# Optimization experiments

Measured on AMD Instinct MI355X. Metric: run time of the kernel, lower is better.

Reference implementation:

```python
import jax, jax.numpy as jnp
import numpy as np


def _sqdist(X1, X2):
    # squared euclidean distance matrix, matches torch.cdist(...,p=2)**2
    d2 = (jnp.sum(X1 * X1, -1)[:, None] + jnp.sum(X2 * X2, -1)[None, :]
          - 2.0 * (X1 @ X2.T))
    return jnp.maximum(d2, 0.0)


def setup_inputs() -> dict:
    key = jax.random.key(0)
    k1, k2, k3, k4, k5, k6 = jax.random.split(key, 6)
    n, m, d, C = 1024, 2048, 4, 64
    X_train = jax.random.normal(k1, (n, d), dtype=jnp.float32)
    y_train = jax.random.normal(k2, (n,), dtype=jnp.float32)
    X_test = jax.random.normal(k3, (m, d), dtype=jnp.float32)
    # positive params within the priors' supports
    lengthscale = jax.random.uniform(k4, (C,), minval=0.1, maxval=3.0, dtype=jnp.float32)
    variance = jax.random.uniform(k5, (C,), minval=0.1, maxval=3.0, dtype=jnp.float32)
    noise = jax.random.uniform(k6, (C,), minval=0.01, maxval=0.5, dtype=jnp.float32)
    return {"X_train": X_train, "y_train": y_train, "X_test": X_test,
            "lengthscale": lengthscale, "variance": variance, "noise": noise}


def reference(X_train, y_train, X_test, lengthscale, variance, noise):
    n = X_train.shape[0]
    ls2 = (lengthscale ** 2)[:, None, None]          # [C,1,1]
    var = variance[:, None, None]                     # [C,1,1]
    d2_tr = _sqdist(X_train, X_train)                 # [n,n]
    d2_te = _sqdist(X_test, X_train)                  # [m,n]
    K_train = var * jnp.exp(-0.5 * d2_tr[None] / ls2)   # [C,n,n]
    K_test = var * jnp.exp(-0.5 * d2_te[None] / ls2)    # [C,m,n]
    K_noisy = K_train + noise[:, None, None] * jnp.eye(n, dtype=K_train.dtype)
    L = jnp.linalg.cholesky(K_noisy)                  # batched [C,n,n]

    def per_chain(Lc, Ktc):
        solve = jax.scipy.linalg.solve_triangular
        z = solve(Lc, y_train, lower=True)            # [n]
        alpha = solve(Lc, z, lower=True, trans=1)     # [n]
        pred_mean = Ktc @ alpha                       # [m]
        v = solve(Lc, Ktc.T, lower=True)              # [n,m]
        pred_var = jnp.sum(v * v, axis=0)             # [m]
        return pred_mean, pred_var

    means, vars_ = jax.vmap(per_chain)(L, K_test)     # [C,m] each
    return means.mean(axis=0), vars_.mean(axis=0)
```

## Files before the change

kernel.cpp:

```cpp
#include <hip/hip_runtime.h>
#include <hip/hip_fp16.h>
#include <math.h>

#define N 1024
#define M 2048
#define C 64
#define NB 128
#define TB 8
#define NBLK 36
#define PL ((size_t)NBLK*NB*NB)

typedef __attribute__((ext_vector_type(8))) short bf16x8;
typedef __attribute__((ext_vector_type(8))) _Float16 f16x8;
typedef __attribute__((ext_vector_type(4))) float f32x4;

__device__ __forceinline__ size_t pblk(int ib, int jt){
    return ((size_t)((ib*(ib+1))/2 + jt))*((size_t)NB*NB);
}

#define TT(r,c) T[(r)][(((c)+(r)) & 127)]


__device__ __forceinline__ float sqdist4(const float4 a, const float4 b){
    float dx=a.x-b.x, dy=a.y-b.y, dz=a.z-b.z, dw=a.w-b.w;
    return dx*dx+dy*dy+dz*dz+dw*dw;
}

__device__ __forceinline__ void split4(float x0, float x1, float x2, float x3,
                                       uint2& hi, uint2& lo){
    unsigned b0=__float_as_uint(x0), b1=__float_as_uint(x1),
             b2=__float_as_uint(x2), b3=__float_as_uint(x3);
    unsigned h0=b0&0xFFFF0000u, h1=b1&0xFFFF0000u, h2=b2&0xFFFF0000u, h3=b3&0xFFFF0000u;
    hi.x = (h0>>16)|h1;  hi.y = (h2>>16)|h3;
    float l0=x0-__uint_as_float(h0), l1=x1-__uint_as_float(h1),
          l2=x2-__uint_as_float(h2), l3=x3-__uint_as_float(h3);
    lo.x = (__float_as_uint(l0)>>16) | (__float_as_uint(l1)&0xFFFF0000u);
    lo.y = (__float_as_uint(l2)>>16) | (__float_as_uint(l3)&0xFFFF0000u);
}

__device__ void chol_invert_lds(float T[NB][NB], int tid){
    for (int j = 0; j < NB; j++){
        float d = TT(j,j);
        float inv = 1.0f / sqrtf(d);
        for (int i = j+1+tid; i < NB; i += 256) TT(i,j) *= inv;
        if (tid == 0) TT(j,j) = d * inv;
        __syncthreads();
        int i = j+1 + (tid >> 1);
        if (i < NB){
            float lij = TT(i,j);
            for (int k = j+1+(tid&1); k <= i; k += 2)
                TT(i,k) -= lij * TT(k,j);
        }
        __syncthreads();
    }
    for (int i = 0; i < NB; i++){
        float inv_ii = 1.0f / TT(i,i);
        int j = tid & 127, hi = tid >> 7;
        float S = 0.0f;
        if (j < i){
            for (int k = i-1-hi; k >= j; k -= 2)
                S += TT(i,k) * TT(k,j);
        }
        if (hi && j < i) TT(j,i) = S;
        __syncthreads();
        if (!hi){
            if (j < i)      TT(i,j) = -inv_ii * (S + TT(j,i));
            else if (j == i) TT(i,i) = inv_ii;
        }
        __syncthreads();
    }
}


struct FragLds { __half Ah[4096], Al[4096], Bh[4096], Bl[4096]; };
struct SmX { float4 xr[NB]; float4 xc[NB]; };
union SmU { FragLds f; float T[NB][NB]; SmX x; };

__device__ __forceinline__ void stage_f16(__half* __restrict__ Hh, __half* __restrict__ Hl,
                                          const float* __restrict__ S, int ld,
                                          int k0, bool contig, int tid){
    #pragma unroll
    for (int h = 0; h < 2; h++){
        int u = tid + h*256;
        int fr = u & 15, kg = (u>>4)&3, rt = (u>>6)&3, hf = u>>8;
        int rc = hf*64 + rt*16 + fr;
        int kk = k0 + kg*8;
        float x[8];
        if (contig){
            float4 v0 = *(const float4*)&S[(size_t)rc*ld + kk];
            float4 v1 = *(const float4*)&S[(size_t)rc*ld + kk + 4];
            x[0]=v0.x;x[1]=v0.y;x[2]=v0.z;x[3]=v0.w;
            x[4]=v1.x;x[5]=v1.y;x[6]=v1.z;x[7]=v1.w;
        } else {
            #pragma unroll
            for (int e=0;e<8;e++) x[e] = S[(size_t)(kk+e)*ld + rc];
        }
        union { __half h[8]; uint4 u4; } Hi, Lo;
        #pragma unroll
        for (int e=0;e<8;e++){
            __half hv = __float2half_rn(x[e]);
            Hi.h[e] = hv;
            Lo.h[e] = __float2half_rn(x[e] - __half2float(hv));
        }
        *(uint4*)&Hh[(size_t)u*8] = Hi.u4;
        *(uint4*)&Hl[(size_t)u*8] = Lo.u4;
    }
}

__device__ __forceinline__ void mfma_slab_f16(const __half* Ah, const __half* Al,
                                              const __half* Bh, const __half* Bl,
                                              int wrow, int wcol, int lane,
                                              f32x4 acc[4][4]){
    f16x8 ah[4], al[4];
    #pragma unroll
    for (int rt=0;rt<4;rt++){
        ah[rt] = *(const f16x8*)&Ah[((size_t)((wrow*4+rt)*64 + lane))*8];
        al[rt] = *(const f16x8*)&Al[((size_t)((wrow*4+rt)*64 + lane))*8];
    }
    #pragma unroll
    for (int ct=0;ct<4;ct++){
        f16x8 bh = *(const f16x8*)&Bh[((size_t)((wcol*4+ct)*64 + lane))*8];
        f16x8 bl = *(const f16x8*)&Bl[((size_t)((wcol*4+ct)*64 + lane))*8];
        #pragma unroll
        for (int rt=0;rt<4;rt++){
            f32x4 a = acc[rt][ct];
            a = __builtin_amdgcn_mfma_f32_16x16x32_f16(ah[rt], bh, a, 0,0,0);
            a = __builtin_amdgcn_mfma_f32_16x16x32_f16(ah[rt], bl, a, 0,0,0);
            a = __builtin_amdgcn_mfma_f32_16x16x32_f16(al[rt], bh, a, 0,0,0);
            acc[rt][ct] = a;
        }
    }
}

__device__ void gemm_f16_unit(const float* __restrict__ A, int lda,
                              const float* __restrict__ B, int ldb, bool bContig,
                              FragLds& F, f32x4 acc[4][4], int tid){
    int lane = tid & 63, w = tid >> 6, wrow = w>>1, wcol = w&1;
    for (int k0 = 0; k0 < NB; k0 += 32){
        __syncthreads();
        stage_f16(F.Ah, F.Al, A, lda, k0, true, tid);
        stage_f16(F.Bh, F.Bl, B, ldb, k0, bContig, tid);
        __syncthreads();
        mfma_slab_f16(F.Ah, F.Al, F.Bh, F.Bl, wrow, wcol, lane, acc);
    }
}

__device__ __forceinline__ void store_f16acc(float* __restrict__ Cp, int ldc,
                                             const f32x4 acc[4][4], float sgn, int tid){
    int lane = tid&63, w = tid>>6, wrow = w>>1, wcol = w&1;
    int fr = lane&15, kg = lane>>4;
    #pragma unroll
    for (int rt=0;rt<4;rt++)
      #pragma unroll
      for (int ct=0;ct<4;ct++)
        #pragma unroll
        for (int r=0;r<4;r++){
            int row = wrow*64 + rt*16 + kg*4 + r;
            int col = wcol*64 + ct*16 + fr;
            Cp[(size_t)row*ldc + col] = sgn*acc[rt][ct][r];
        }
}

#define ZERO_ACC(acc) { _Pragma("unroll") for (int zi=0;zi<4;zi++) _Pragma("unroll") for (int zj=0;zj<4;zj++) acc[zi][zj] = (f32x4)0.0f; }


__global__ void k_init_acc(float* __restrict__ acc){
    int i = blockIdx.x*blockDim.x + threadIdx.x;
    if (i < 2*M) acc[i] = 0.0f;
}

__global__ void k_build_d2te(const float* __restrict__ Xtr, const float* __restrict__ Xte,
                             float* __restrict__ d2){
    int j = blockIdx.x;
    float4 xj = ((const float4*)Xte)[j];
    for (int i = threadIdx.x; i < N; i += blockDim.x){
        float4 xi = ((const float4*)Xtr)[i];
        d2[(size_t)j*N + i] = sqdist4(xi,xj);
    }
}

__global__ void k_final(const float* __restrict__ acc, float* __restrict__ out){
    int i = blockIdx.x*blockDim.x + threadIdx.x;
    if (i < 2*M) out[i] = acc[i] * (1.0f/64.0f);
}

__global__ __launch_bounds__(256) void k_build_K(const float* __restrict__ Xtr,
                          const float* __restrict__ ls,
                          const float* __restrict__ var, const float* __restrict__ noise,
                          float* __restrict__ Lbuf){
    __shared__ SmU sm;
    int c = blockIdx.y, flat = blockIdx.x;
    int ib = 0; while ((ib+1)*(ib+2)/2 <= flat) ib++;
    int jt = flat - ib*(ib+1)/2;
    int tid = threadIdx.x;
    if (tid < NB) sm.x.xr[tid] = ((const float4*)Xtr)[ib*NB + tid];
    else          sm.x.xc[tid-NB] = ((const float4*)Xtr)[jt*NB + (tid-NB)];
    __syncthreads();
    float il2 = 1.0f/(ls[c]*ls[c]);
    float vc = var[c], nc = noise[c];
    float* blk = Lbuf + c*PL + pblk(ib,jt);
    for (int idx = tid; idx < NB*NB; idx += 256){
        int r = idx >> 7, col = idx & 127;
        float d2v = sqdist4(sm.x.xr[r], sm.x.xc[col]);
        float v = vc*__expf(-0.5f*d2v*il2);
        if (ib==jt && r==col) v += nc;
        blk[idx] = v;
    }
    if (flat == 0){
        __threadfence_block();
        __syncthreads();
        float (*T)[NB] = sm.T;
        for (int idx = tid; idx < NB*NB; idx += 256){
            int r = idx >> 7, col = idx & 127;
            TT(r,col) = blk[idx];
        }
        __syncthreads();
        chol_invert_lds(T, tid);
        for (int idx = tid; idx < NB*NB; idx += 256){
            int r = idx >> 7, col = idx & 127;
            blk[idx] = (col <= r) ? TT(r,col) : 0.0f;
        }
    }
}

__global__ __launch_bounds__(256) void k_panel(float* __restrict__ Lbuf, int kb){
    __shared__ FragLds F;
    int c = blockIdx.x;
    int ib = kb + 1 + blockIdx.y;
    int tid = threadIdx.x;
    float* base = Lbuf + (size_t)c*PL;
    float* Ablk = base + pblk(ib,kb);
    const float* Dv = base + pblk(kb,kb);
    f32x4 acc[4][4]; ZERO_ACC(acc);
    gemm_f16_unit(Ablk, NB, Dv, NB, true, F, acc, tid);
    store_f16acc(Ablk, NB, acc, 1.0f, tid);
}

__global__ __launch_bounds__(256) void k_syrk(float* __restrict__ Lbuf, int kb){
    __shared__ SmU sm;
    int c = blockIdx.x;
    int flat = blockIdx.y;
    int di = 0; while ((di+1)*(di+2)/2 <= flat) di++;
    int dj = flat - di*(di+1)/2;
    int i = kb+1+di, j = kb+1+dj;
    int tid = threadIdx.x;
    float* base = Lbuf + (size_t)c*PL;
    float* Cblk = base + pblk(i,j);
    const float* Ablk = base + pblk(i,kb);
    const float* Bblk = base + pblk(j,kb);
    f32x4 acc[4][4]; ZERO_ACC(acc);
    gemm_f16_unit(Ablk, NB, Bblk, NB, true, sm.f, acc, tid);
    int lane = tid&63, w = tid>>6, wrow = w>>1, wcol = w&1;
    int fr = lane&15, kg = lane>>4;
    if (flat != 0){
        #pragma unroll
        for (int rt=0;rt<4;rt++)
          #pragma unroll
          for (int ct=0;ct<4;ct++)
            #pragma unroll
            for (int r=0;r<4;r++){
                int row = wrow*64 + rt*16 + kg*4 + r;
                int col = wcol*64 + ct*16 + fr;
                Cblk[(size_t)row*NB + col] -= acc[rt][ct][r];
            }
    } else {
        __syncthreads();
        float (*T)[NB] = sm.T;
        #pragma unroll
        for (int rt=0;rt<4;rt++)
          #pragma unroll
          for (int ct=0;ct<4;ct++)
            #pragma unroll
            for (int r=0;r<4;r++){
                int row = wrow*64 + rt*16 + kg*4 + r;
                int col = wcol*64 + ct*16 + fr;
                TT(row,col) = Cblk[(size_t)row*NB + col] - acc[rt][ct][r];
            }
        __syncthreads();
        chol_invert_lds(T, tid);
        for (int idx = tid; idx < NB*NB; idx += 256){
            int r = idx >> 7, col = idx & 127;
            Cblk[idx] = (col <= r) ? TT(r,col) : 0.0f;
        }
    }
}

__global__ __launch_bounds__(256) void k_gemmA(float* __restrict__ Trow,
                                               const float* __restrict__ Lbuf, int ib){
    __shared__ FragLds F;
    int c = blockIdx.x, ct = blockIdx.y;
    int tid = threadIdx.x;
    const float* base = Lbuf + (size_t)c*PL;
    const float* Dv = base + pblk(ib,ib);
    const float* Bsrc = base + pblk(ib,ct);
    f32x4 acc[4][4]; ZERO_ACC(acc);
    gemm_f16_unit(Dv, NB, Bsrc, NB, false, F, acc, tid);
    store_f16acc(Trow + (size_t)c*NB*N + ct*NB, N, acc, 1.0f, tid);
}

__global__ __launch_bounds__(256) void k_gemmB(float* __restrict__ Lbuf,
                                               const float* __restrict__ Trow, int ib){
    __shared__ FragLds F;
    int c = blockIdx.x, jt = blockIdx.y;
    int tid = threadIdx.x;
    const float* G = Trow + (size_t)c*NB*N;
    float* base = Lbuf + (size_t)c*PL;
    f32x4 acc[4][4]; ZERO_ACC(acc);
    for (int kt = jt; kt < ib; kt++)
        gemm_f16_unit(G + kt*NB, N, base + pblk(kt,jt), NB, false, F, acc, tid);
    store_f16acc(base + pblk(ib,jt), NB, acc, -1.0f, tid);
}

__global__ void k_zvec(const float* __restrict__ Lbuf, const float* __restrict__ y,
                       float* __restrict__ z){
    int c = blockIdx.x;
    int p = blockIdx.y * 4 + (threadIdx.x >> 6);
    int lane = threadIdx.x & 63;
    int pb = p >> 7, pl = p & 127;
    const float* base = Lbuf + (size_t)c*PL;
    float s = 0.0f;
    for (int kt = 0; kt <= pb; kt++){
        const float* row = base + pblk(pb,kt) + (size_t)pl*NB;
        int lim = (kt==pb) ? pl : NB-1;
        for (int i = lane; i <= lim; i += 64) s += row[i]*y[kt*NB + i];
    }
    for (int off = 32; off; off >>= 1) s += __shfl_down(s, off);
    if (lane == 0) z[c*N + p] = s;
}

__global__ __launch_bounds__(256) void k_wsplit(float* __restrict__ Lbuf){
    int c = blockIdx.y, flat = blockIdx.x;
    int tid = threadIdx.x;
    float* blk = Lbuf + c*PL + (size_t)flat*NB*NB;
    float4 v[16];
    #pragma unroll
    for (int h = 0; h < 8; h++){
        int g = tid + h*256;
        int u = g & 511, slab = g >> 9;
        int fr = u&15, kg = (u>>4)&3, rt = (u>>6)&3, hf = u>>8;
        int row = hf*64 + rt*16 + fr;
        int k = slab*32 + kg*8;
        v[2*h]   = *(const float4*)&blk[(size_t)row*NB + k];
        v[2*h+1] = *(const float4*)&blk[(size_t)row*NB + k + 4];
    }
    __syncthreads();
    unsigned short* out = (unsigned short*)blk;
    #pragma unroll
    for (int h = 0; h < 8; h++){
        int g = tid + h*256;
        int u = g & 511, slab = g >> 9;
        uint2 h0, l0, h1, l1;
        split4(v[2*h].x, v[2*h].y, v[2*h].z, v[2*h].w, h0, l0);
        split4(v[2*h+1].x, v[2*h+1].y, v[2*h+1].z, v[2*h+1].w, h1, l1);
        *(uint4*)&out[((size_t)(slab*2+0)*512 + u)*8] = make_uint4(h0.x,h0.y,h1.x,h1.y);
        *(uint4*)&out[((size_t)(slab*2+1)*512 + u)*8] = make_uint4(l0.x,l0.y,l1.x,l1.y);
    }
}

__global__ __launch_bounds__(256) void k_bigg(const float* __restrict__ Lbuf,
                                              const float* __restrict__ d2,
                                              const float* __restrict__ zbuf,
                                              const float* __restrict__ ls,
                                              const float* __restrict__ var,
                                              float* __restrict__ acc_out){
    __shared__ unsigned short Ah[4096], Al[4096], Bh[4096], Bl[4096];
    int flat = blockIdx.x, c = blockIdx.y;
    int jt = flat & 15;
    int pt = ((flat >> 4) + (jt & 7)) & 7;
    int tid = threadIdx.x;
    int lane = tid & 63, w = tid >> 6;
    int wrow = w >> 1, wcol = w & 1;
    float il2 = 1.0f/(ls[c]*ls[c]);
    float vc = var[c];
    float ec = -0.5f*il2;
    const float* Arow = d2 + (size_t)(jt*NB)*N;
    const float* Wbase = Lbuf + (size_t)c*PL;
    int klen = (pt+1)*NB;
    f32x4 acc[4][4]; ZERO_ACC(acc);

    int fr = lane & 15, kg = lane >> 4;
    int q = tid & 7, rs = tid >> 3;
    int kgq = q >> 1, e4 = (q & 1) * 4;

    for (int k0 = 0; k0 < klen; k0 += 32){
        const unsigned short* Wimg = (const unsigned short*)(Wbase + pblk(pt, k0 >> 7));
        int slab = (k0 & 127) >> 5;
        const unsigned short* hi_img = Wimg + (size_t)(slab*2+0)*4096;
        const unsigned short* lo_img = Wimg + (size_t)(slab*2+1)*4096;
        __syncthreads();
        #pragma unroll
        for (int p = 0; p < 4; p++){
            int row = rs + 32*p;
            float4 dv = *(const float4*)&Arow[(size_t)row*N + k0 + q*4];
            float x0 = __expf(ec*dv.x), x1 = __expf(ec*dv.y);
            float x2 = __expf(ec*dv.z), x3 = __expf(ec*dv.w);
            uint2 hi, lo; split4(x0,x1,x2,x3, hi, lo);
            int u = (row&15) + kgq*16 + ((row>>4)&3)*64 + (row>>6)*256;
            *(uint2*)&Ah[(size_t)u*8 + e4] = hi;
            *(uint2*)&Al[(size_t)u*8 + e4] = lo;
        }
        #pragma unroll
        for (int h2 = 0; h2 < 2; h2++){
            int u = tid + h2*256;
            *(uint4*)&Bh[(size_t)u*8] = *(const uint4*)&hi_img[(size_t)u*8];
            *(uint4*)&Bl[(size_t)u*8] = *(const uint4*)&lo_img[(size_t)u*8];
        }
        __syncthreads();
        bf16x8 ah[4], al[4];
        #pragma unroll
        for (int rt=0;rt<4;rt++){
            ah[rt] = *(const bf16x8*)&Ah[((size_t)((wrow*4+rt)*64 + lane))*8];
            al[rt] = *(const bf16x8*)&Al[((size_t)((wrow*4+rt)*64 + lane))*8];
        }
        #pragma unroll
        for (int ct=0;ct<4;ct++){
            bf16x8 bh = *(const bf16x8*)&Bh[((size_t)((wcol*4+ct)*64 + lane))*8];
            bf16x8 bl = *(const bf16x8*)&Bl[((size_t)((wcol*4+ct)*64 + lane))*8];
            #pragma unroll
            for (int rt=0;rt<4;rt++){
                f32x4 a = acc[rt][ct];
                a = __builtin_amdgcn_mfma_f32_16x16x32_bf16(ah[rt], bh, a, 0,0,0);
                a = __builtin_amdgcn_mfma_f32_16x16x32_bf16(ah[rt], bl, a, 0,0,0);
                a = __builtin_amdgcn_mfma_f32_16x16x32_bf16(al[rt], bh, a, 0,0,0);
                acc[rt][ct] = a;
            }
        }
    }
    float vc2 = vc*vc;
    float zv[4];
    #pragma unroll
    for (int ct=0;ct<4;ct++) zv[ct] = zbuf[c*N + pt*NB + wcol*64 + ct*16 + fr];
    #pragma unroll
    for (int rt=0;rt<4;rt++){
        #pragma unroll
        for (int r=0;r<4;r++){
            float m = 0.0f, v = 0.0f;
            #pragma unroll
            for (int ct=0;ct<4;ct++){
                float x = acc[rt][ct][r];
                v += x*x; m += x*zv[ct];
            }
            m += __shfl_xor(m, 1);  v += __shfl_xor(v, 1);
            m += __shfl_xor(m, 2);  v += __shfl_xor(v, 2);
            m += __shfl_xor(m, 4);  v += __shfl_xor(v, 4);
            m += __shfl_xor(m, 8);  v += __shfl_xor(v, 8);
            if (fr == 0){
                int j = jt*NB + wrow*64 + rt*16 + kg*4 + r;
                atomicAdd(&acc_out[j], vc*m);
                atomicAdd(&acc_out[M + j], vc2*v);
            }
        }
    }
}


extern "C" void kernel_launch(void* const* d_in, const int* in_sizes, int n_in,
                              void* d_out, int out_size, void* d_ws, size_t ws_size,
                              hipStream_t stream) {
    const float* Xtr = (const float*)d_in[0];
    const float* ytr = (const float*)d_in[1];
    const float* Xte = (const float*)d_in[2];
    const float* ls  = (const float*)d_in[3];
    const float* var = (const float*)d_in[4];
    const float* noi = (const float*)d_in[5];
    float* out = (float*)d_out;

    float* ws = (float*)d_ws;
    const size_t shared_fl  = (size_t)N*M + 2*M;
    const size_t perchain   = PL + (size_t)NB*N + (size_t)N;
    size_t avail = ws_size / sizeof(float);
    if (avail < shared_fl + perchain) return;
    int Gmax = (int)((avail - shared_fl) / perchain);
    if (Gmax > C) Gmax = C;
    int nbatch = (C + Gmax - 1) / Gmax;
    int G = (C + nbatch - 1) / nbatch;

    float* d2te = ws;
    float* acc  = d2te + (size_t)N*M;
    float* Lbuf = acc  + 2*M;
    float* Trow = Lbuf + (size_t)G*PL;
    float* zbuf = Trow + (size_t)G*NB*N;

    k_init_acc<<<dim3((2*M+255)/256), dim3(256), 0, stream>>>(acc);
    k_build_d2te<<<dim3(M), dim3(256), 0, stream>>>(Xtr, Xte, d2te);

    for (int c0 = 0; c0 < C; c0 += G){
        int g = C - c0 < G ? C - c0 : G;

        k_build_K<<<dim3(NBLK, g), dim3(256), 0, stream>>>(Xtr, ls+c0, var+c0, noi+c0, Lbuf);

        for (int kb = 0; kb < TB-1; kb++){
            int rem = TB-1-kb;
            k_panel<<<dim3(g, rem), dim3(256), 0, stream>>>(Lbuf, kb);
            k_syrk<<<dim3(g, rem*(rem+1)/2), dim3(256), 0, stream>>>(Lbuf, kb);
        }
        for (int ib = 1; ib < TB; ib++){
            k_gemmA<<<dim3(g, ib), dim3(256), 0, stream>>>(Trow, Lbuf, ib);
            k_gemmB<<<dim3(g, ib), dim3(256), 0, stream>>>(Lbuf, Trow, ib);
        }
        k_zvec<<<dim3(g, N/4), dim3(256), 0, stream>>>(Lbuf, ytr, zbuf);
        k_wsplit<<<dim3(NBLK, g), dim3(256), 0, stream>>>(Lbuf);
        k_bigg<<<dim3(128, g), dim3(256), 0, stream>>>(Lbuf, d2te, zbuf, ls+c0, var+c0, acc);
    }
    k_final<<<dim3((2*M+255)/256), dim3(256), 0, stream>>>(acc, out);
}
```

Baseline: 5.498 ms.

## Fuse z-vector computation into wsplit and read B fragments from global

The separate k_zvec launch is removed. Its triangular matrix-vector product now runs inside k_wsplit, with one block per 128x128 tile adding its partial row sums into zbuf via atomicAdd; k_build_K zeroes zbuf beforehand. Separately, k_bigg no longer copies the pre-split hi/lo weight images into LDS and instead loads the bf16 fragments straight from global memory inside the MFMA loop. This cuts a launch, LDS traffic and LDS footprint, but risks exposed global-load latency in the inner loop. The fused z path also sums the full diagonal block, so it is correct only if the upper triangle of each diagonal block is zero.

Result: no change. 5.597 ms (+1.8%).

```diff
diff --git a/kernel.cpp b/kernel.cpp
--- a/kernel.cpp
+++ b/kernel.cpp
@@ -187,12 +187,13 @@
 __global__ __launch_bounds__(256) void k_build_K(const float* __restrict__ Xtr,
                           const float* __restrict__ ls,
                           const float* __restrict__ var, const float* __restrict__ noise,
-                          float* __restrict__ Lbuf){
+                          float* __restrict__ Lbuf, float* __restrict__ zbuf){
     __shared__ SmU sm;
     int c = blockIdx.y, flat = blockIdx.x;
     int ib = 0; while ((ib+1)*(ib+2)/2 <= flat) ib++;
     int jt = flat - ib*(ib+1)/2;
     int tid = threadIdx.x;
+    if (flat < TB && tid < NB) zbuf[c*N + flat*NB + tid] = 0.0f;
     if (tid < NB) sm.x.xr[tid] = ((const float4*)Xtr)[ib*NB + tid];
     else          sm.x.xc[tid-NB] = ((const float4*)Xtr)[jt*NB + (tid-NB)];
     __syncthreads();
@@ -311,27 +312,23 @@
     store_f16acc(base + pblk(ib,jt), NB, acc, -1.0f, tid);
 }
 
-__global__ void k_zvec(const float* __restrict__ Lbuf, const float* __restrict__ y,
-                       float* __restrict__ z){
-    int c = blockIdx.x;
-    int p = blockIdx.y * 4 + (threadIdx.x >> 6);
-    int lane = threadIdx.x & 63;
-    int pb = p >> 7, pl = p & 127;
-    const float* base = Lbuf + (size_t)c*PL;
-    float s = 0.0f;
-    for (int kt = 0; kt <= pb; kt++){
-        const float* row = base + pblk(pb,kt) + (size_t)pl*NB;
-        int lim = (kt==pb) ? pl : NB-1;
-        for (int i = lane; i <= lim; i += 64) s += row[i]*y[kt*NB + i];
-    }
-    for (int off = 32; off; off >>= 1) s += __shfl_down(s, off);
-    if (lane == 0) z[c*N + p] = s;
-}
-
-__global__ __launch_bounds__(256) void k_wsplit(float* __restrict__ Lbuf){
+__global__ __launch_bounds__(256) void k_wsplit(float* __restrict__ Lbuf,
+                                                const float* __restrict__ ytr,
+                                                float* __restrict__ zbuf){
     int c = blockIdx.y, flat = blockIdx.x;
+    int pb = 0; while ((pb+1)*(pb+2)/2 <= flat) pb++;
+    int kt = flat - pb*(pb+1)/2;
     int tid = threadIdx.x;
     float* blk = Lbuf + c*PL + (size_t)flat*NB*NB;
+    {
+        int row = tid >> 1, half = tid & 1;
+        const float* wp = blk + (size_t)row*NB + half*64;
+        const float* yp = ytr + kt*NB + half*64;
+        float s = 0.0f;
+        for (int i = 0; i < 64; i++) s += wp[i]*yp[i];
+        s += __shfl_xor(s, 1);
+        if (!half) atomicAdd(&zbuf[c*N + pb*NB + row], s);
+    }
     float4 v[16];
     #pragma unroll
     for (int h = 0; h < 8; h++){
@@ -363,7 +360,7 @@
                                               const float* __restrict__ ls,
                                               const float* __restrict__ var,
                                               float* __restrict__ acc_out){
-    __shared__ unsigned short Ah[4096], Al[4096], Bh[4096], Bl[4096];
+    __shared__ unsigned short Ah[4096], Al[4096];
     int flat = blockIdx.x, c = blockIdx.y;
     int jt = flat & 15;
     int pt = ((flat >> 4) + (jt & 7)) & 7;
@@ -399,12 +396,6 @@
             *(uint2*)&Ah[(size_t)u*8 + e4] = hi;
             *(uint2*)&Al[(size_t)u*8 + e4] = lo;
         }
-        #pragma unroll
-        for (int h2 = 0; h2 < 2; h2++){
-            int u = tid + h2*256;
-            *(uint4*)&Bh[(size_t)u*8] = *(const uint4*)&hi_img[(size_t)u*8];
-            *(uint4*)&Bl[(size_t)u*8] = *(const uint4*)&lo_img[(size_t)u*8];
-        }
         __syncthreads();
         bf16x8 ah[4], al[4];
         #pragma unroll
@@ -414,8 +405,8 @@
         }
         #pragma unroll
         for (int ct=0;ct<4;ct++){
-            bf16x8 bh = *(const bf16x8*)&Bh[((size_t)((wcol*4+ct)*64 + lane))*8];
-            bf16x8 bl = *(const bf16x8*)&Bl[((size_t)((wcol*4+ct)*64 + lane))*8];
+            bf16x8 bh = *(const bf16x8*)&hi_img[((size_t)((wcol*4+ct)*64 + lane))*8];
+            bf16x8 bl = *(const bf16x8*)&lo_img[((size_t)((wcol*4+ct)*64 + lane))*8];
             #pragma unroll
             for (int rt=0;rt<4;rt++){
                 f32x4 a = acc[rt][ct];
@@ -487,7 +478,7 @@
     for (int c0 = 0; c0 < C; c0 += G){
         int g = C - c0 < G ? C - c0 : G;
 
-        k_build_K<<<dim3(NBLK, g), dim3(256), 0, stream>>>(Xtr, ls+c0, var+c0, noi+c0, Lbuf);
+        k_build_K<<<dim3(NBLK, g), dim3(256), 0, stream>>>(Xtr, ls+c0, var+c0, noi+c0, Lbuf, zbuf);
 
         for (int kb = 0; kb < TB-1; kb++){
             int rem = TB-1-kb;
@@ -498,8 +489,7 @@
             k_gemmA<<<dim3(g, ib), dim3(256), 0, stream>>>(Trow, Lbuf, ib);
             k_gemmB<<<dim3(g, ib), dim3(256), 0, stream>>>(Lbuf, Trow, ib);
         }
-        k_zvec<<<dim3(g, N/4), dim3(256), 0, stream>>>(Lbuf, ytr, zbuf);
-        k_wsplit<<<dim3(NBLK, g), dim3(256), 0, stream>>>(Lbuf);
+        k_wsplit<<<dim3(NBLK, g), dim3(256), 0, stream>>>(Lbuf, ytr, zbuf);
         k_bigg<<<dim3(128, g), dim3(256), 0, stream>>>(Lbuf, d2te, zbuf, ls+c0, var+c0, acc);
     }
     k_final<<<dim3((2*M+255)/256), dim3(256), 0, stream>>>(acc, out);
```
